# Performance work log

Measured on AMD Instinct MI355X. Metric: run time of the kernel, lower is better.

Reference implementation:

```python
import jax, jax.numpy as jnp
import numpy as np

T, B, N, D, H = 4, 16, 1024, 512, 8
DECAY, THR = 0.9, 1.0
SURR_ALPHA = 2.0  # sigmoid surrogate-gradient sharpness


@jax.custom_vjp
def spike(u):
    # Heaviside spike with sigmoid surrogate gradient.
    return (u >= 0.0).astype(u.dtype)

def _spike_fwd(u):
    return (u >= 0.0).astype(u.dtype), u

def _spike_bwd(u, g):
    s = jax.nn.sigmoid(SURR_ALPHA * u)
    return (g * SURR_ALPHA * s * (1.0 - s),)

spike.defvjp(_spike_fwd, _spike_bwd)


def lif(x):
    # x: (T, M, D). Membrane recurrence over time with soft reset.
    def step(mem, xt):
        mem = mem * DECAY + xt
        s = spike(mem - THR)
        return mem - s * THR, s
    _, spikes = jax.lax.scan(step, jnp.zeros_like(x[0]), x)
    return spikes  # (T, M, D), binary


def setup_inputs() -> dict:
    key = jax.random.key(0)
    ks = jax.random.split(key, 5)
    sc = D ** -0.5
    return {
        "x_seq": jax.random.normal(ks[0], (T, B, N, D), jnp.float32),
        "Wq": jax.random.normal(ks[1], (D, D), jnp.float32) * sc,
        "Wk": jax.random.normal(ks[2], (D, D), jnp.float32) * sc,
        "Wv": jax.random.normal(ks[3], (D, D), jnp.float32) * sc,
        "Wp": jax.random.normal(ks[4], (D, D), jnp.float32) * sc,
        "bp": jnp.zeros((D,), jnp.float32),
    }


def reference(x_seq, Wq, Wk, Wv, Wp, bp):
    Tn, Bn, Nn, Dn = x_seq.shape
    Hd = Dn // H
    xf = x_seq.reshape(Tn, Bn * Nn, Dn)
    # torch's .view(T, B, H, N, Hd) on a contiguous (T, B*N, D) tensor is a
    # raw row-major reshape; jnp.reshape matches it exactly.
    q = lif(xf @ Wq.T).reshape(Tn, Bn, H, Nn, Hd)
    k = lif(xf @ Wk.T).reshape(Tn, Bn, H, Nn, Hd)
    v = lif(xf @ Wv.T).reshape(Tn, Bn, H, Nn, Hd)
    kv = k * v
    context = jnp.cumsum(kv, axis=0)  # linear-attention carry over timesteps
    out = (q * context).reshape(Tn, Bn * Nn, Dn)
    out = out @ Wp.T + bp
    return out.reshape(Tn, Bn, Nn, Dn)
```

## Files before the change

### kernel.cpp

```cpp
#include <hip/hip_runtime.h>
#include <hip/hip_bf16.h>
#include <stdint.h>


#define T_ 4
#define M_ 16384
#define D_ 512
#define MT 64
#define DT 32
#define BK 32
#define RS 40
#define RS2 36
#define TAU 5e-4f
#define NKS 48

typedef __attribute__((ext_vector_type(8))) short bs8;
typedef __attribute__((ext_vector_type(4))) float f32x4;
typedef unsigned short u16;

static __device__ __forceinline__ void split1(float f, u16& h, u16& l) {
  __hip_bfloat16 hb = __float2bfloat16(f);
  float hf = __bfloat162float(hb);
  __hip_bfloat16 lb = __float2bfloat16(f - hf);
  h = __builtin_bit_cast(u16, hb);
  l = __builtin_bit_cast(u16, lb);
}
static __device__ __forceinline__ uint32_t pack2(u16 a, u16 b) {
  return (uint32_t)a | ((uint32_t)b << 16);
}
static __device__ __forceinline__ uint32_t packf2(float a, float b) {
  return (__builtin_bit_cast(uint32_t, a) >> 16) |
         (__builtin_bit_cast(uint32_t, b) & 0xFFFF0000u);
}

__global__ void zero_count(uint32_t* c) { *c = 0; }

__global__ void conv_wp(const float* __restrict__ Wp, u16* __restrict__ wpb) {
  int i = (blockIdx.x * 256 + threadIdx.x) * 8;
  float4 a = *reinterpret_cast<const float4*>(Wp + i);
  float4 b = *reinterpret_cast<const float4*>(Wp + i + 4);
  u16 h[8];
  h[0] = __builtin_bit_cast(u16, __float2bfloat16(a.x));
  h[1] = __builtin_bit_cast(u16, __float2bfloat16(a.y));
  h[2] = __builtin_bit_cast(u16, __float2bfloat16(a.z));
  h[3] = __builtin_bit_cast(u16, __float2bfloat16(a.w));
  h[4] = __builtin_bit_cast(u16, __float2bfloat16(b.x));
  h[5] = __builtin_bit_cast(u16, __float2bfloat16(b.y));
  h[6] = __builtin_bit_cast(u16, __float2bfloat16(b.z));
  h[7] = __builtin_bit_cast(u16, __float2bfloat16(b.w));
  uint4 o;
  o.x = pack2(h[0], h[1]); o.y = pack2(h[2], h[3]);
  o.z = pack2(h[4], h[5]); o.w = pack2(h[6], h[7]);
  *reinterpret_cast<uint4*>(wpb + i) = o;
}

__global__ __launch_bounds__(256)
void xsplit(const float* __restrict__ x, u16* __restrict__ xh,
            u16* __restrict__ xl) {
  size_t flat = ((size_t)blockIdx.x * 256 + threadIdx.x) * 8;
  int k = (int)(flat & 511);
  int m = (int)((flat >> 9) & 16383);
  int t = (int)(flat >> 23);
  float4 a = *reinterpret_cast<const float4*>(x + flat);
  float4 b = *reinterpret_cast<const float4*>(x + flat + 4);
  u16 h[8], l[8];
  split1(a.x,h[0],l[0]); split1(a.y,h[1],l[1]);
  split1(a.z,h[2],l[2]); split1(a.w,h[3],l[3]);
  split1(b.x,h[4],l[4]); split1(b.y,h[5],l[5]);
  split1(b.z,h[6],l[6]); split1(b.w,h[7],l[7]);
  size_t dst = (((size_t)t * 16 + (k >> 5)) * 16384 + m) * 32 + (k & 31);
  uint4 oh = make_uint4(pack2(h[0],h[1]), pack2(h[2],h[3]),
                        pack2(h[4],h[5]), pack2(h[6],h[7]));
  uint4 ol = make_uint4(pack2(l[0],l[1]), pack2(l[2],l[3]),
                        pack2(l[4],l[5]), pack2(l[6],l[7]));
  *reinterpret_cast<uint4*>(xh + dst) = oh;
  *reinterpret_cast<uint4*>(xl + dst) = ol;
}

__global__ __launch_bounds__(256)
void wsplit(const float* __restrict__ Wq, const float* __restrict__ Wk,
            const float* __restrict__ Wv, u16* __restrict__ wh,
            u16* __restrict__ wl) {
  size_t flat = ((size_t)blockIdx.x * 256 + threadIdx.x) * 8;
  int k = (int)(flat & 511);
  int d = (int)((flat >> 9) & 511);
  int mat = (int)(flat >> 18);
  const float* wp = (mat == 0) ? Wq : ((mat == 1) ? Wk : Wv);
  size_t src = ((size_t)d << 9) + k;
  float4 a = *reinterpret_cast<const float4*>(wp + src);
  float4 b = *reinterpret_cast<const float4*>(wp + src + 4);
  u16 h[8], l[8];
  split1(a.x,h[0],l[0]); split1(a.y,h[1],l[1]);
  split1(a.z,h[2],l[2]); split1(a.w,h[3],l[3]);
  split1(b.x,h[4],l[4]); split1(b.y,h[5],l[5]);
  split1(b.z,h[6],l[6]); split1(b.w,h[7],l[7]);
  size_t dst = (((size_t)mat * 16 + (k >> 5)) * 512 + d) * 32 + (k & 31);
  uint4 oh = make_uint4(pack2(h[0],h[1]), pack2(h[2],h[3]),
                        pack2(h[4],h[5]), pack2(h[6],h[7]));
  uint4 ol = make_uint4(pack2(l[0],l[1]), pack2(l[2],l[3]),
                        pack2(l[4],l[5]), pack2(l[6],l[7]));
  *reinterpret_cast<uint4*>(wh + dst) = oh;
  *reinterpret_cast<uint4*>(wl + dst) = ol;
}

__global__ __launch_bounds__(256, 3)
void qkv_mfma_lif3(const u16* __restrict__ xh, const u16* __restrict__ xl,
                   const u16* __restrict__ wh, const u16* __restrict__ wl,
                   uint8_t* __restrict__ s_out,
                   uint32_t* __restrict__ count,
                   uint32_t* __restrict__ list,
                   uint32_t cap) {
  __shared__ u16 Xs[2][T_][MT][RS2];
  __shared__ u16 Wsh[2][3][DT][RS2];
  const int tid = threadIdx.x;
  const int lane = tid & 63;
  const int w = tid >> 6;

  const int sblk = blockIdx.x;
  const int xcd = sblk & 7, q = sblk >> 3;
  const int c_mt = xcd + 8 * (q >> 4);
  const int jdb = q & 15;
  const int d0 = jdb * DT;
  const int m0 = c_mt * MT;

  f32x4 acc[T_][3][2];
  #pragma unroll
  for (int t = 0; t < T_; ++t)
    #pragma unroll
    for (int mat = 0; mat < 3; ++mat)
      #pragma unroll
      for (int dh = 0; dh < 2; ++dh) acc[t][mat][dh] = (f32x4)0.0f;

  uint4 ra[4];
  uint2 rb[3];

#define ISSUE(ks_)                                                           \
  {                                                                          \
    int seg = (ks_) >> 4, kk = (ks_) & 15;                                   \
    const u16* xsrc = (seg == 1) ? xl : xh;                                  \
    _Pragma("unroll")                                                        \
    for (int c = 0; c < 4; ++c) {                                            \
      int idx = c * 256 + tid;                                               \
      int t = idx >> 8, r = idx & 255;                                       \
      int m = r >> 2, kc = r & 3;                                            \
      ra[c] = *reinterpret_cast<const uint4*>(                               \
          xsrc + (((size_t)t * 16 + kk) * 16384 + m0 + m) * 32 + kc * 8);    \
    }                                                                        \
    const u16* wsrc = (seg == 2) ? wl : wh;                                  \
    _Pragma("unroll")                                                        \
    for (int c = 0; c < 3; ++c) {                                            \
      int idx = c * 256 + tid;                                               \
      int mat = idx >> 8, r = idx & 255;                                     \
      int dd = r >> 3, kq = r & 7;                                           \
      rb[c] = *reinterpret_cast<const uint2*>(                               \
          wsrc + (((size_t)mat * 16 + kk) * 512 + d0 + dd) * 32 + kq * 4);   \
    }                                                                        \
  }

#define STORE(buf_)                                                          \
  {                                                                          \
    _Pragma("unroll")                                                        \
    for (int c = 0; c < 4; ++c) {                                            \
      int idx = c * 256 + tid;                                               \
      int t = idx >> 8, r = idx & 255;                                       \
      int m = r >> 2, kc = r & 3;                                            \
      *reinterpret_cast<uint4*>(&Xs[buf_][t][m][kc * 8]) = ra[c];            \
    }                                                                        \
    _Pragma("unroll")                                                        \
    for (int c = 0; c < 3; ++c) {                                            \
      int idx = c * 256 + tid;                                               \
      int mat = idx >> 8, r = idx & 255;                                     \
      int dd = r >> 3, kq = r & 7;                                           \
      *reinterpret_cast<uint2*>(&Wsh[buf_][mat][dd][kq * 4]) = rb[c];        \
    }                                                                        \
  }

  ISSUE(0);
  STORE(0);
  __syncthreads();

  for (int ks = 0; ks < NKS; ++ks) {
    const int buf = ks & 1;
    if (ks + 1 < NKS) ISSUE(ks + 1);

    bs8 a[T_];
    #pragma unroll
    for (int t = 0; t < T_; ++t)
      a[t] = *reinterpret_cast<const bs8*>(
          &Xs[buf][t][w * 16 + (lane & 15)][(lane >> 4) * 8]);
    #pragma unroll
    for (int mat = 0; mat < 3; ++mat) {
      bs8 b0 = *reinterpret_cast<const bs8*>(
          &Wsh[buf][mat][(lane & 15)][(lane >> 4) * 8]);
      bs8 b1 = *reinterpret_cast<const bs8*>(
          &Wsh[buf][mat][16 + (lane & 15)][(lane >> 4) * 8]);
      #pragma unroll
      for (int t = 0; t < T_; ++t) {
        acc[t][mat][0] = __builtin_amdgcn_mfma_f32_16x16x32_bf16(
            a[t], b0, acc[t][mat][0], 0, 0, 0);
        acc[t][mat][1] = __builtin_amdgcn_mfma_f32_16x16x32_bf16(
            a[t], b1, acc[t][mat][1], 0, 0, 0);
      }
    }

    if (ks + 1 < NKS) STORE(buf ^ 1);
    __syncthreads();
  }
#undef ISSUE
#undef STORE

  const int rbase = w * 16 + ((lane >> 4) << 2);
  const int dd = lane & 15;
  #pragma unroll
  for (int dh = 0; dh < 2; ++dh) {
    const int gd = d0 + dh * 16 + dd;
    #pragma unroll
    for (int r = 0; r < 4; ++r) {
      const int gm = m0 + rbase + r;
      float mq = 0.f, mk = 0.f, mv = 0.f;
      int ctx = 0; bool flag = false;
      #pragma unroll
      for (int t = 0; t < T_; ++t) {
        mq = mq * 0.9f + acc[t][0][dh][r];
        mk = mk * 0.9f + acc[t][1][dh][r];
        mv = mv * 0.9f + acc[t][2][dh][r];
        flag |= (fabsf(mq - 1.f) < TAU) || (fabsf(mk - 1.f) < TAU) ||
                (fabsf(mv - 1.f) < TAU);
        int sq = (mq >= 1.f); int sk = (mk >= 1.f); int sv = (mv >= 1.f);
        mq -= (float)sq; mk -= (float)sk; mv -= (float)sv;
        ctx += sk & sv;
        s_out[(size_t)t * (M_ * (size_t)D_) + (size_t)gm * D_ + gd] =
            (uint8_t)(sq ? ctx : 0);
      }
      if (flag) {
        uint32_t pos = atomicAdd(count, 1u);
        if (pos < cap) list[pos] = ((uint32_t)gm << 9) | (uint32_t)gd;
      }
    }
  }
}

__global__ __launch_bounds__(256, 2)
void qkv_mfma_lif(const float* __restrict__ x,
                  const float* __restrict__ Wq,
                  const float* __restrict__ Wk,
                  const float* __restrict__ Wv,
                  uint8_t* __restrict__ s_out,
                  uint32_t* __restrict__ count,
                  uint32_t* __restrict__ list,
                  uint32_t cap) {
  __shared__ u16 Xh[T_][MT][RS], Xl[T_][MT][RS];
  __shared__ u16 Wh[3][DT][RS], Wl[3][DT][RS];
  const int tid = threadIdx.x;
  const int lane = tid & 63;
  const int w = tid >> 6;
  const int d0 = blockIdx.x * DT;
  const int m0 = blockIdx.y * MT;

  f32x4 acc[T_][3][2];
  #pragma unroll
  for (int t = 0; t < T_; ++t)
    #pragma unroll
    for (int mat = 0; mat < 3; ++mat)
      #pragma unroll
      for (int dh = 0; dh < 2; ++dh) acc[t][mat][dh] = (f32x4)0.0f;

  for (int k0 = 0; k0 < D_; k0 += BK) {
    __syncthreads();
    #pragma unroll
    for (int c = 0; c < 8; ++c) {
      int idx = c * 256 + tid;
      int k4 = idx & 7, row = idx >> 3;
      int t = row >> 6, m = row & 63;
      float4 f = *reinterpret_cast<const float4*>(
          x + ((size_t)t * M_ + (size_t)(m0 + m)) * D_ + k0 + k4 * 4);
      u16 h0,h1,h2,h3,l0,l1,l2,l3;
      split1(f.x,h0,l0); split1(f.y,h1,l1); split1(f.z,h2,l2); split1(f.w,h3,l3);
      *reinterpret_cast<uint2*>(&Xh[t][m][k4*4]) = make_uint2(pack2(h0,h1), pack2(h2,h3));
      *reinterpret_cast<uint2*>(&Xl[t][m][k4*4]) = make_uint2(pack2(l0,l1), pack2(l2,l3));
    }
    #pragma unroll
    for (int c = 0; c < 3; ++c) {
      int idx = c * 256 + tid;
      int k4 = idx & 7, row = idx >> 3;
      int mat = row >> 5, dd = row & 31;
      const float* wp = (mat == 0) ? Wq : ((mat == 1) ? Wk : Wv);
      float4 f = *reinterpret_cast<const float4*>(
          wp + (size_t)(d0 + dd) * D_ + k0 + k4 * 4);
      u16 h0,h1,h2,h3,l0,l1,l2,l3;
      split1(f.x,h0,l0); split1(f.y,h1,l1); split1(f.z,h2,l2); split1(f.w,h3,l3);
      *reinterpret_cast<uint2*>(&Wh[mat][dd][k4*4]) = make_uint2(pack2(h0,h1), pack2(h2,h3));
      *reinterpret_cast<uint2*>(&Wl[mat][dd][k4*4]) = make_uint2(pack2(l0,l1), pack2(l2,l3));
    }
    __syncthreads();

    bs8 a[T_][2];
    #pragma unroll
    for (int t = 0; t < T_; ++t) {
      a[t][0] = *reinterpret_cast<const bs8*>(&Xh[t][w*16 + (lane&15)][(lane>>4)*8]);
      a[t][1] = *reinterpret_cast<const bs8*>(&Xl[t][w*16 + (lane&15)][(lane>>4)*8]);
    }
    #pragma unroll
    for (int mat = 0; mat < 3; ++mat) {
      bs8 b[2][2];
      #pragma unroll
      for (int dh = 0; dh < 2; ++dh) {
        b[dh][0] = *reinterpret_cast<const bs8*>(&Wh[mat][dh*16 + (lane&15)][(lane>>4)*8]);
        b[dh][1] = *reinterpret_cast<const bs8*>(&Wl[mat][dh*16 + (lane&15)][(lane>>4)*8]);
      }
      #pragma unroll
      for (int t = 0; t < T_; ++t)
        #pragma unroll
        for (int dh = 0; dh < 2; ++dh) {
          acc[t][mat][dh] = __builtin_amdgcn_mfma_f32_16x16x32_bf16(
              a[t][0], b[dh][0], acc[t][mat][dh], 0, 0, 0);
          acc[t][mat][dh] = __builtin_amdgcn_mfma_f32_16x16x32_bf16(
              a[t][0], b[dh][1], acc[t][mat][dh], 0, 0, 0);
          acc[t][mat][dh] = __builtin_amdgcn_mfma_f32_16x16x32_bf16(
              a[t][1], b[dh][0], acc[t][mat][dh], 0, 0, 0);
        }
    }
  }

  const int rbase = w * 16 + ((lane >> 4) << 2);
  const int dd = lane & 15;
  #pragma unroll
  for (int dh = 0; dh < 2; ++dh) {
    const int gd = d0 + dh * 16 + dd;
    #pragma unroll
    for (int r = 0; r < 4; ++r) {
      const int gm = m0 + rbase + r;
      float mq = 0.f, mk = 0.f, mv = 0.f;
      int ctx = 0; bool flag = false;
      #pragma unroll
      for (int t = 0; t < T_; ++t) {
        mq = mq * 0.9f + acc[t][0][dh][r];
        mk = mk * 0.9f + acc[t][1][dh][r];
        mv = mv * 0.9f + acc[t][2][dh][r];
        flag |= (fabsf(mq - 1.f) < TAU) || (fabsf(mk - 1.f) < TAU) ||
                (fabsf(mv - 1.f) < TAU);
        int sq = (mq >= 1.f); int sk = (mk >= 1.f); int sv = (mv >= 1.f);
        mq -= (float)sq; mk -= (float)sk; mv -= (float)sv;
        ctx += sk & sv;
        s_out[(size_t)t * (M_ * (size_t)D_) + (size_t)gm * D_ + gd] =
            (uint8_t)(sq ? ctx : 0);
      }
      if (flag) {
        uint32_t pos = atomicAdd(count, 1u);
        if (pos < cap) list[pos] = ((uint32_t)gm << 9) | (uint32_t)gd;
      }
    }
  }
}

__global__ __launch_bounds__(64, 8)
void fix_borderline(const float* __restrict__ x,
                    const float* __restrict__ Wq,
                    const float* __restrict__ Wk,
                    const float* __restrict__ Wv,
                    uint8_t* __restrict__ s_out,
                    const uint32_t* __restrict__ count,
                    const uint32_t* __restrict__ list,
                    uint32_t cap) {
  uint32_t n = *count; if (n > cap) n = cap;
  const int lane = threadIdx.x;
  for (uint32_t j = blockIdx.x; j < n; j += gridDim.x) {
    uint32_t e = list[j];
    int m = (int)(e >> 9), d = (int)(e & 511);
    const int kb = lane * 8;
    float xr[T_][8], wr[3][8];
    #pragma unroll
    for (int t = 0; t < T_; ++t) {
      float4 a = *reinterpret_cast<const float4*>(x + ((size_t)t*M_ + m)*D_ + kb);
      float4 b = *reinterpret_cast<const float4*>(x + ((size_t)t*M_ + m)*D_ + kb + 4);
      xr[t][0]=a.x; xr[t][1]=a.y; xr[t][2]=a.z; xr[t][3]=a.w;
      xr[t][4]=b.x; xr[t][5]=b.y; xr[t][6]=b.z; xr[t][7]=b.w;
    }
    #pragma unroll
    for (int mat = 0; mat < 3; ++mat) {
      const float* wp = (mat == 0) ? Wq : ((mat == 1) ? Wk : Wv);
      float4 a = *reinterpret_cast<const float4*>(wp + (size_t)d*D_ + kb);
      float4 b = *reinterpret_cast<const float4*>(wp + (size_t)d*D_ + kb + 4);
      wr[mat][0]=a.x; wr[mat][1]=a.y; wr[mat][2]=a.z; wr[mat][3]=a.w;
      wr[mat][4]=b.x; wr[mat][5]=b.y; wr[mat][6]=b.z; wr[mat][7]=b.w;
    }
    double pd[T_][3];
    #pragma unroll
    for (int t = 0; t < T_; ++t)
      #pragma unroll
      for (int mat = 0; mat < 3; ++mat) {
        double s = 0.0;
        #pragma unroll
        for (int i = 0; i < 8; ++i) s += (double)xr[t][i] * (double)wr[mat][i];
        pd[t][mat] = s;
      }
    #pragma unroll
    for (int off = 32; off > 0; off >>= 1)
      #pragma unroll
      for (int t = 0; t < T_; ++t)
        #pragma unroll
        for (int mat = 0; mat < 3; ++mat)
          pd[t][mat] += __shfl_xor(pd[t][mat], off);
    double mq = 0.0, mk = 0.0, mv = 0.0;
    int ctx = 0; uint8_t sv4[T_];
    #pragma unroll
    for (int t = 0; t < T_; ++t) {
      mq = mq * 0.9 + pd[t][0];
      mk = mk * 0.9 + pd[t][1];
      mv = mv * 0.9 + pd[t][2];
      int sq = (mq >= 1.0); int sk = (mk >= 1.0); int sv = (mv >= 1.0);
      mq -= (double)sq; mk -= (double)sk; mv -= (double)sv;
      ctx += sk & sv;
      sv4[t] = (uint8_t)(sq ? ctx : 0);
    }
    if (lane < T_)
      s_out[(size_t)lane * (M_ * (size_t)D_) + (size_t)m * D_ + d] = sv4[lane];
  }
}

__global__ __launch_bounds__(256, 4)
void out_gemm_mfma(const uint8_t* __restrict__ s,
                   const u16* __restrict__ wpb,
                   const float* __restrict__ bp,
                   float* __restrict__ out) {
  __shared__ u16 As[128][BK];
  __shared__ u16 Bs[64][BK];
  const int tid = threadIdx.x;
  const int lane = tid & 63;
  const int w = tid >> 6;
  const int j0 = blockIdx.x * 64;
  const int r0 = blockIdx.y * 128;

  f32x4 acc[2][4];
  #pragma unroll
  for (int rg = 0; rg < 2; ++rg)
    #pragma unroll
    for (int jf = 0; jf < 4; ++jf) acc[rg][jf] = (f32x4)0.0f;

  for (int k0 = 0; k0 < D_; k0 += BK) {
    __syncthreads();
    {
      int row = tid >> 1, half = tid & 1;
      uint4 u = *reinterpret_cast<const uint4*>(
          s + (size_t)(r0 + row) * D_ + k0 + half * 16);
      uint32_t dw[4] = {u.x, u.y, u.z, u.w};
      uint32_t pk[8];
      #pragma unroll
      for (int qq = 0; qq < 4; ++qq) {
        uint32_t v = dw[qq];
        float f0 = (float)(v & 0xff);
        float f1 = (float)((v >> 8) & 0xff);
        float f2 = (float)((v >> 16) & 0xff);
        float f3 = (float)(v >> 24);
        pk[qq*2+0] = packf2(f0, f1);
        pk[qq*2+1] = packf2(f2, f3);
      }
      uint4* dst = reinterpret_cast<uint4*>(&As[row][half * 16]);
      dst[0] = make_uint4(pk[0], pk[1], pk[2], pk[3]);
      dst[1] = make_uint4(pk[4], pk[5], pk[6], pk[7]);
    }
    {
      int row = tid >> 2, qq = tid & 3;
      uint4 u = *reinterpret_cast<const uint4*>(
          wpb + (size_t)(j0 + row) * D_ + k0 + qq * 8);
      *reinterpret_cast<uint4*>(&Bs[row][qq * 8]) = u;
    }
    __syncthreads();

    const int rb = w * 32;
    bs8 a0 = *reinterpret_cast<const bs8*>(&As[rb      + (lane&15)][(lane>>4)*8]);
    bs8 a1 = *reinterpret_cast<const bs8*>(&As[rb + 16 + (lane&15)][(lane>>4)*8]);
    #pragma unroll
    for (int jf = 0; jf < 4; ++jf) {
      bs8 b = *reinterpret_cast<const bs8*>(&Bs[jf*16 + (lane&15)][(lane>>4)*8]);
      acc[0][jf] = __builtin_amdgcn_mfma_f32_16x16x32_bf16(a0, b, acc[0][jf], 0, 0, 0);
      acc[1][jf] = __builtin_amdgcn_mfma_f32_16x16x32_bf16(a1, b, acc[1][jf], 0, 0, 0);
    }
  }

  const int col = lane & 15;
  const int rloc = (lane >> 4) * 4;
  #pragma unroll
  for (int jf = 0; jf < 4; ++jf) {
    float bv = bp[j0 + jf * 16 + col];
    #pragma unroll
    for (int rg = 0; rg < 2; ++rg) {
      #pragma unroll
      for (int reg = 0; reg < 4; ++reg) {
        out[(size_t)(r0 + w * 32 + rg * 16 + rloc + reg) * D_ +
            j0 + jf * 16 + col] = acc[rg][jf][reg] + bv;
      }
    }
  }
}

extern "C" void kernel_launch(void* const* d_in, const int* in_sizes, int n_in,
                              void* d_out, int out_size, void* d_ws, size_t ws_size,
                              hipStream_t stream) {
  const float* x  = (const float*)d_in[0];
  const float* Wq = (const float*)d_in[1];
  const float* Wk = (const float*)d_in[2];
  const float* Wv = (const float*)d_in[3];
  const float* Wp = (const float*)d_in[4];
  const float* bp = (const float*)d_in[5];
  float* out = (float*)d_out;

  const size_t s_bytes    = (size_t)T_ * M_ * D_;
  const size_t wp_bytes   = (size_t)D_ * D_ * sizeof(u16);
  const size_t list_bytes = (size_t)4 << 20;
  const size_t xp_bytes   = (size_t)T_ * M_ * D_ * sizeof(u16);
  const size_t wl_bytes   = (size_t)3 * D_ * D_ * sizeof(u16);

  char* p = (char*)d_ws;
  uint8_t*  s_ws  = (uint8_t*)p;              p += s_bytes;
  u16*      wpb   = (u16*)p;                  p += wp_bytes;
  uint32_t* count = (uint32_t*)p;             p += 64;
  uint32_t* list  = (uint32_t*)p;             p += list_bytes;
  size_t head = (size_t)(p - (char*)d_ws);
  uint32_t cap = (uint32_t)(list_bytes / sizeof(uint32_t));
  if (ws_size < head) cap = 0;

  const size_t need_full = head + 2 * xp_bytes + 2 * wl_bytes;

  zero_count<<<1, 1, 0, stream>>>(count);
  conv_wp<<<dim3(128), dim3(256), 0, stream>>>(Wp, wpb);

  if (ws_size >= need_full) {
    u16* xhp = (u16*)p;                       p += xp_bytes;
    u16* xlp = (u16*)p;                       p += xp_bytes;
    u16* whp = (u16*)p;                       p += wl_bytes;
    u16* wlp = (u16*)p;
    xsplit<<<dim3(16384), dim3(256), 0, stream>>>(x, xhp, xlp);
    wsplit<<<dim3(384), dim3(256), 0, stream>>>(Wq, Wk, Wv, whp, wlp);
    qkv_mfma_lif3<<<dim3(4096), dim3(256), 0, stream>>>(
        xhp, xlp, whp, wlp, s_ws, count, list, cap);
  } else {
    qkv_mfma_lif<<<dim3(D_/DT, M_/MT), dim3(256), 0, stream>>>(
        x, Wq, Wk, Wv, s_ws, count, list, cap);
  }
  fix_borderline<<<dim3(1024), dim3(64), 0, stream>>>(
      x, Wq, Wk, Wv, s_ws, count, list, cap);
  out_gemm_mfma<<<dim3(D_/64, (T_*M_)/128), dim3(256), 0, stream>>>(
      s_ws, wpb, bp, out);
}
```

Baseline: 636.4 us.

## Deepen QKV GEMM prefetch to two stages with register double-buffering

```diff
diff --git a/kernel.cpp b/kernel.cpp
--- a/kernel.cpp
+++ b/kernel.cpp
@@ -103,7 +103,7 @@
   *reinterpret_cast<uint4*>(wl + dst) = ol;
 }
 
-__global__ __launch_bounds__(256, 3)
+__global__ __launch_bounds__(256, 2)
 void qkv_mfma_lif3(const u16* __restrict__ xh, const u16* __restrict__ xl,
                    const u16* __restrict__ wh, const u16* __restrict__ wl,
                    uint8_t* __restrict__ s_out,
@@ -131,10 +131,9 @@
       #pragma unroll
       for (int dh = 0; dh < 2; ++dh) acc[t][mat][dh] = (f32x4)0.0f;
 
-  uint4 ra[4];
-  uint2 rb[3];
-
-#define ISSUE(ks_)                                                           \
+  uint4 raA[4], raB[4], rbA[2], rbB[2];
+
+#define ISSUE(ks_, ra_, rb_)                                                 \
   {                                                                          \
     int seg = (ks_) >> 4, kk = (ks_) & 15;                                   \
     const u16* xsrc = (seg == 1) ? xl : xh;                                  \
@@ -143,71 +142,84 @@
       int idx = c * 256 + tid;                                               \
       int t = idx >> 8, r = idx & 255;                                       \
       int m = r >> 2, kc = r & 3;                                            \
-      ra[c] = *reinterpret_cast<const uint4*>(                               \
+      ra_[c] = *reinterpret_cast<const uint4*>(                              \
           xsrc + (((size_t)t * 16 + kk) * 16384 + m0 + m) * 32 + kc * 8);    \
     }                                                                        \
     const u16* wsrc = (seg == 2) ? wl : wh;                                  \
-    _Pragma("unroll")                                                        \
-    for (int c = 0; c < 3; ++c) {                                            \
-      int idx = c * 256 + tid;                                               \
-      int mat = idx >> 8, r = idx & 255;                                     \
-      int dd = r >> 3, kq = r & 7;                                           \
-      rb[c] = *reinterpret_cast<const uint2*>(                               \
-          wsrc + (((size_t)mat * 16 + kk) * 512 + d0 + dd) * 32 + kq * 4);   \
+    {                                                                        \
+      int mat = tid >> 7, r = tid & 127, dd = r >> 2, kc = r & 3;            \
+      rb_[0] = *reinterpret_cast<const uint4*>(                              \
+          wsrc + (((size_t)mat * 16 + kk) * 512 + d0 + dd) * 32 + kc * 8);   \
+      if (tid < 128) {                                                       \
+        int dd1 = tid >> 2, kc1 = tid & 3;                                   \
+        rb_[1] = *reinterpret_cast<const uint4*>(                            \
+            wsrc + (((size_t)2 * 16 + kk) * 512 + d0 + dd1) * 32 + kc1 * 8); \
+      }                                                                      \
     }                                                                        \
   }
 
-#define STORE(buf_)                                                          \
+#define STOREM(buf_, ra_, rb_)                                               \
   {                                                                          \
     _Pragma("unroll")                                                        \
     for (int c = 0; c < 4; ++c) {                                            \
       int idx = c * 256 + tid;                                               \
       int t = idx >> 8, r = idx & 255;                                       \
       int m = r >> 2, kc = r & 3;                                            \
-      *reinterpret_cast<uint4*>(&Xs[buf_][t][m][kc * 8]) = ra[c];            \
+      *reinterpret_cast<uint4*>(&Xs[buf_][t][m][kc * 8]) = ra_[c];           \
     }                                                                        \
+    {                                                                        \
+      int mat = tid >> 7, r = tid & 127, dd = r >> 2, kc = r & 3;            \
+      *reinterpret_cast<uint4*>(&Wsh[buf_][mat][dd][kc * 8]) = rb_[0];       \
+      if (tid < 128) {                                                       \
+        int dd1 = tid >> 2, kc1 = tid & 3;                                   \
+        *reinterpret_cast<uint4*>(&Wsh[buf_][2][dd1][kc1 * 8]) = rb_[1];     \
+      }                                                                      \
+    }                                                                        \
+  }
+
+#define COMPUTE(buf_)                                                        \
+  {                                                                          \
+    bs8 afr[T_];                                                             \
     _Pragma("unroll")                                                        \
-    for (int c = 0; c < 3; ++c) {                                            \
-      int idx = c * 256 + tid;                                               \
-      int mat = idx >> 8, r = idx & 255;                                     \
-      int dd = r >> 3, kq = r & 7;                                           \
-      *reinterpret_cast<uint2*>(&Wsh[buf_][mat][dd][kq * 4]) = rb[c];        \
+    for (int t = 0; t < T_; ++t)                                             \
+      afr[t] = *reinterpret_cast<const bs8*>(                                \
+          &Xs[buf_][t][w * 16 + (lane & 15)][(lane >> 4) * 8]);              \
+    _Pragma("unroll")                                                        \
+    for (int mat = 0; mat < 3; ++mat) {                                      \
+      bs8 b0 = *reinterpret_cast<const bs8*>(                                \
+          &Wsh[buf_][mat][(lane & 15)][(lane >> 4) * 8]);                    \
+      bs8 b1 = *reinterpret_cast<const bs8*>(                                \
+          &Wsh[buf_][mat][16 + (lane & 15)][(lane >> 4) * 8]);               \
+      __builtin_amdgcn_s_setprio(1);                                         \
+      _Pragma("unroll")                                                      \
+      for (int t = 0; t < T_; ++t) {                                         \
+        acc[t][mat][0] = __builtin_amdgcn_mfma_f32_16x16x32_bf16(            \
+            afr[t], b0, acc[t][mat][0], 0, 0, 0);                            \
+        acc[t][mat][1] = __builtin_amdgcn_mfma_f32_16x16x32_bf16(            \
+            afr[t], b1, acc[t][mat][1], 0, 0, 0);                            \
+      }                                                                      \
+      __builtin_amdgcn_s_setprio(0);                                         \
     }                                                                        \
   }
 
-  ISSUE(0);
-  STORE(0);
+  ISSUE(0, raA, rbA);
+  ISSUE(1, raB, rbB);
+  STOREM(0, raA, rbA);
   __syncthreads();
 
-  for (int ks = 0; ks < NKS; ++ks) {
-    const int buf = ks & 1;
-    if (ks + 1 < NKS) ISSUE(ks + 1);
-
-    bs8 a[T_];
-    #pragma unroll
-    for (int t = 0; t < T_; ++t)
-      a[t] = *reinterpret_cast<const bs8*>(
-          &Xs[buf][t][w * 16 + (lane & 15)][(lane >> 4) * 8]);
-    #pragma unroll
-    for (int mat = 0; mat < 3; ++mat) {
-      bs8 b0 = *reinterpret_cast<const bs8*>(
-          &Wsh[buf][mat][(lane & 15)][(lane >> 4) * 8]);
-      bs8 b1 = *reinterpret_cast<const bs8*>(
-          &Wsh[buf][mat][16 + (lane & 15)][(lane >> 4) * 8]);
-      #pragma unroll
-      for (int t = 0; t < T_; ++t) {
-        acc[t][mat][0] = __builtin_amdgcn_mfma_f32_16x16x32_bf16(
-            a[t], b0, acc[t][mat][0], 0, 0, 0);
-        acc[t][mat][1] = __builtin_amdgcn_mfma_f32_16x16x32_bf16(
-            a[t], b1, acc[t][mat][1], 0, 0, 0);
-      }
-    }
-
-    if (ks + 1 < NKS) STORE(buf ^ 1);
+  for (int ks = 0; ks < NKS; ks += 2) {
+    if (ks + 2 < NKS) ISSUE(ks + 2, raA, rbA);
+    COMPUTE(0);
+    STOREM(1, raB, rbB);
     __syncthreads();
+    if (ks + 3 < NKS) ISSUE(ks + 3, raB, rbB);
+    COMPUTE(1);
+    if (ks + 2 < NKS) STOREM(0, raA, rbA);
+    __syncthreads();
   }
 #undef ISSUE
-#undef STORE
+#undef STOREM
+#undef COMPUTE
 
   const int rbase = w * 16 + ((lane >> 4) << 2);
   const int dd = lane & 15;
```

Result: slower. 1.713 ms (+169.1%).
